# Performance work log

Hardware: AMD Instinct MI355X
Metric: run time of the kernel (lower is better)

Reference implementation:

```python
import jax, jax.numpy as jnp
import numpy as np

DIM = 256
HEADS = 8
HEAD_DIM = DIM // HEADS
SCALE = HEAD_DIM ** -0.5
B, N = 2048, 49
NW = 64


def setup_inputs() -> dict:
    key = jax.random.key(0)
    ks = jax.random.split(key, 7)
    x = jax.random.normal(ks[0], (B, N, DIM), dtype=jnp.float32)
    mask = jax.random.normal(ks[1], (NW, N + 1, N + 1), dtype=jnp.float32)
    class_token = 0.02 * jax.random.normal(ks[2], (1, 1, DIM), dtype=jnp.float32)
    qkv_w = jax.random.normal(ks[3], (DIM, 3 * DIM), dtype=jnp.float32) / np.sqrt(DIM)
    qkv_b = jnp.zeros((3 * DIM,), dtype=jnp.float32)
    proj_w = jax.random.normal(ks[4], (DIM, DIM), dtype=jnp.float32) / np.sqrt(DIM)
    proj_b = jnp.zeros((DIM,), dtype=jnp.float32)
    return {"x": x, "mask": mask, "class_token": class_token,
            "qkv_w": qkv_w, "qkv_b": qkv_b, "proj_w": proj_w, "proj_b": proj_b}


def reference(x, mask, class_token, qkv_w, qkv_b, proj_w, proj_b):
    b, n, c = x.shape
    n1 = n + 1
    # prepend learnable class token
    cls = jnp.broadcast_to(class_token, (b, 1, c))
    xc = jnp.concatenate([cls, x], axis=1)  # (B, N+1, C)
    # fused qkv projection
    qkv = xc @ qkv_w + qkv_b                 # (B, N+1, 3C)
    qkv = qkv.reshape(b, n1, 3, HEADS, HEAD_DIM)
    qkv = jnp.transpose(qkv, (2, 0, 3, 1, 4))  # (3, B, H, N+1, Dh)
    q, k, v = qkv[0] * SCALE, qkv[1], qkv[2]
    attn = jnp.einsum('bhid,bhjd->bhij', q, k)  # (B, H, N+1, N+1)
    # per-window additive mask bias
    nw = mask.shape[0]
    attn = attn.reshape(b // nw, nw, HEADS, n1, n1) + mask[None, :, None]
    attn = attn.reshape(b, HEADS, n1, n1)
    attn = jax.nn.softmax(attn, axis=-1)
    out = jnp.einsum('bhij,bhjd->bhid', attn, v)      # (B, H, N+1, Dh)
    out = jnp.transpose(out, (0, 2, 1, 3)).reshape(b, n1, c)
    out = out @ proj_w + proj_b
    return out[:, 0], out[:, 1:]
```

## Files before the change

### kernel.cpp

```cpp
#include <hip/hip_runtime.h>

#define NB    2048
#define N1    50
#define DIMC  256
#define NHEAD 8

typedef short  s16x8 __attribute__((ext_vector_type(8)));
typedef short  s16x4 __attribute__((ext_vector_type(4)));
typedef float  f32x4 __attribute__((ext_vector_type(4)));
typedef float  f32x2 __attribute__((ext_vector_type(2)));

__device__ __forceinline__ unsigned short f2bf(float f) {
    unsigned int u = __builtin_bit_cast(unsigned int, f);
    u = (u + 0x7FFFu + ((u >> 16) & 1u)) >> 16;
    return (unsigned short)u;
}
__device__ __forceinline__ s16x8 ld8(const unsigned short* p) {
    return *(const s16x8*)p;
}
__device__ __forceinline__ void gll16(const unsigned short* g, unsigned short* l) {
    __builtin_amdgcn_global_load_lds(
        (const __attribute__((address_space(1))) unsigned int*)g,
        (__attribute__((address_space(3))) unsigned int*)l, 16, 0, 0);
}

__global__ void prep_kernel(const float* __restrict__ qkv_w, const float* __restrict__ proj_w,
                            const float* __restrict__ mask,
                            unsigned short* __restrict__ wqkvB, unsigned short* __restrict__ wprojB,
                            float* __restrict__ maskP) {
    int idx = blockIdx.x * 256 + threadIdx.x;
    {
        int wv = idx >> 12, q = (idx >> 6) & 63, k = idx & 63;
        float v = (k < 50) ? ((q < 50) ? mask[(wv * 50 + q) * 50 + k] : 0.f) : -1e30f;
        maskP[idx] = v;
    }
    if (idx < 196608) {
        int ks = idx / 24576, rem = idx - ks * 24576, n = rem >> 5, kk = rem & 31;
        wqkvB[idx] = f2bf(qkv_w[(ks * 32 + kk) * 768 + n]);
    }
    if (idx < 65536) {
        int ks = idx >> 13, rem = idx & 8191, n = rem >> 5, kk = rem & 31;
        wprojB[idx] = f2bf(proj_w[(ks * 32 + kk) * 256 + n]);
    }
}

__global__ __launch_bounds__(1024, 4) void attn_kernel(
        const float* __restrict__ x, const float* __restrict__ cls,
        const float* __restrict__ qkv_b, const unsigned short* __restrict__ wqkvB,
        const float* __restrict__ maskP, unsigned short* __restrict__ attO) {
    __shared__ __align__(16) char smem_raw[155648];
    unsigned short* S   = (unsigned short*)smem_raw;
    unsigned short* sQ  = S;
    unsigned short* sK  = S + 20480;
    unsigned short* sVT = S + 40960;
    unsigned short* sP  = S + 59392;
    unsigned short* sXC = S;
    unsigned short* sB0 = S + 16896;
    unsigned short* sB1 = S + 41472;

    const int b = blockIdx.x, tid = threadIdx.x;
    const int lane = tid & 63, w = tid >> 6;
    const int ln15 = lane & 15, quad = lane >> 4, q8 = quad * 8;
    const int wm = w & 1, wn = w >> 1;
    const int win = b & 63;
    const float SCALE = 0.17677669529663687f;

    #pragma unroll
    for (int i = 0; i < 8; ++i) {
        int p = i * 1024 + tid;
        int r = p >> 7, c = (p & 127) * 2;
        float v0, v1;
        if (r == 0)       { v0 = cls[c]; v1 = cls[c + 1]; }
        else if (r <= 49) { const float* px = &x[((size_t)b * 49 + (r - 1)) * 256 + c];
                            f32x2 t = *(const f32x2*)px; v0 = t[0]; v1 = t[1]; }
        else              { v0 = 0.f; v1 = 0.f; }
        *(unsigned int*)&sXC[r * 264 + c] = (unsigned int)f2bf(v0) | ((unsigned int)f2bf(v1) << 16);
    }
    #pragma unroll
    for (int i = 0; i < 3; ++i) {
        int sb = w * 192 + i * 64;
        gll16(wqkvB + (sb + lane) * 8, sB0 + sb * 8);
    }
    __syncthreads();

    f32x4 acc[2][6];
    #pragma unroll
    for (int mt = 0; mt < 2; ++mt)
        #pragma unroll
        for (int nt = 0; nt < 6; ++nt) acc[mt][nt] = f32x4{0.f, 0.f, 0.f, 0.f};

    for (int ks = 0; ks < 8; ++ks) {
        unsigned short* bb = (ks & 1) ? sB1 : sB0;
        if (ks < 7) {
            unsigned short* nb = (ks & 1) ? sB0 : sB1;
            const unsigned short* src = wqkvB + (ks + 1) * 24576;
            #pragma unroll
            for (int i = 0; i < 3; ++i) {
                int sb = w * 192 + i * 64;
                gll16(src + (sb + lane) * 8, nb + sb * 8);
            }
        }
        s16x8 af[2], bf[6];
        #pragma unroll
        for (int mt = 0; mt < 2; ++mt)
            af[mt] = ld8(&sXC[(wm * 32 + mt * 16 + ln15) * 264 + ks * 32 + q8]);
        #pragma unroll
        for (int nt = 0; nt < 6; ++nt)
            bf[nt] = ld8(&bb[(wn * 96 + nt * 16 + ln15) * 32 + q8]);
        #pragma unroll
        for (int mt = 0; mt < 2; ++mt)
            #pragma unroll
            for (int nt = 0; nt < 6; ++nt)
                acc[mt][nt] = __builtin_amdgcn_mfma_f32_16x16x32_bf16(af[mt], bf[nt], acc[mt][nt], 0, 0, 0);
        __syncthreads();
    }

    #pragma unroll
    for (int mt = 0; mt < 2; ++mt) {
        const int tokb = wm * 32 + mt * 16 + quad * 4;
        #pragma unroll
        for (int nt = 0; nt < 6; ++nt) {
            const int gc = wn * 96 + nt * 16 + ln15;
            const int type = gc >> 8;
            const int hd = (gc >> 5) & 7, dd = gc & 31;
            const float bias = qkv_b[gc];
            if (type == 0) {
                #pragma unroll
                for (int i = 0; i < 4; ++i)
                    sQ[hd * 2560 + (tokb + i) * 40 + dd] = f2bf((acc[mt][nt][i] + bias) * SCALE);
            } else if (type == 1) {
                #pragma unroll
                for (int i = 0; i < 4; ++i)
                    sK[hd * 2560 + (tokb + i) * 40 + dd] = f2bf(acc[mt][nt][i] + bias);
            } else {
                s16x4 pk;
                #pragma unroll
                for (int i = 0; i < 4; ++i) pk[i] = f2bf(acc[mt][nt][i] + bias);
                *(s16x4*)&sVT[hd * 2304 + dd * 72 + tokb] = pk;
            }
        }
    }
    __syncthreads();

    const int h = w >> 1, rh = w & 1, qt0 = rh * 2;
    unsigned short* sPw = sP + w * 1152;

    s16x8 ak[4];
    #pragma unroll
    for (int kt = 0; kt < 4; ++kt)
        ak[kt] = ld8(&sK[h * 2560 + (kt * 16 + ln15) * 40 + q8]);

    f32x4 st[2][4];
    #pragma unroll
    for (int mt = 0; mt < 2; ++mt) {
        s16x8 bq = ld8(&sQ[h * 2560 + ((qt0 + mt) * 16 + ln15) * 40 + q8]);
        #pragma unroll
        for (int kt = 0; kt < 4; ++kt) {
            f32x4 z = {0.f, 0.f, 0.f, 0.f};
            st[mt][kt] = __builtin_amdgcn_mfma_f32_16x16x32_bf16(ak[kt], bq, z, 0, 0, 0);
        }
    }
    s16x8 pb[2][2];
    #pragma unroll
    for (int mt = 0; mt < 2; ++mt) {
        float sum = 0.f;
        #pragma unroll
        for (int kt = 0; kt < 4; ++kt) {
            f32x4 mk = *(const f32x4*)&maskP[((size_t)(win * 64 + (qt0 + mt) * 16 + ln15)) * 64 + kt * 16 + quad * 4];
            #pragma unroll
            for (int i = 0; i < 4; ++i) {
                float e = __expf(st[mt][kt][i] + mk[i]);
                st[mt][kt][i] = e;
                sum += e;
            }
        }
        sum += __shfl_xor(sum, 16, 64);
        sum += __shfl_xor(sum, 32, 64);
        const float inv = 1.f / sum;
        #pragma unroll
        for (int kt = 0; kt < 4; ++kt) {
            s16x4 pk;
            #pragma unroll
            for (int i = 0; i < 4; ++i) pk[i] = f2bf(st[mt][kt][i] * inv);
            *(s16x4*)&sPw[ln15 * 72 + kt * 16 + quad * 4] = pk;
        }
        asm volatile("s_waitcnt lgkmcnt(0)" ::: "memory");
        pb[mt][0] = ld8(&sPw[ln15 * 72 + q8]);
        pb[mt][1] = ld8(&sPw[ln15 * 72 + 32 + q8]);
    }
    s16x8 av[2][2];
    #pragma unroll
    for (int dt = 0; dt < 2; ++dt)
        #pragma unroll
        for (int kk = 0; kk < 2; ++kk)
            av[dt][kk] = ld8(&sVT[h * 2304 + (dt * 16 + ln15) * 72 + kk * 32 + q8]);
    f32x4 o[2][2];
    #pragma unroll
    for (int mt = 0; mt < 2; ++mt)
        #pragma unroll
        for (int dt = 0; dt < 2; ++dt) o[mt][dt] = f32x4{0.f, 0.f, 0.f, 0.f};
    #pragma unroll
    for (int mt = 0; mt < 2; ++mt)
        #pragma unroll
        for (int dt = 0; dt < 2; ++dt)
            #pragma unroll
            for (int kk = 0; kk < 2; ++kk)
                o[mt][dt] = __builtin_amdgcn_mfma_f32_16x16x32_bf16(av[dt][kk], pb[mt][kk], o[mt][dt], 0, 0, 0);
    #pragma unroll
    for (int mt = 0; mt < 2; ++mt) {
        const int qg = (qt0 + mt) * 16 + ln15;
        if (qg < N1) {
            #pragma unroll
            for (int dt = 0; dt < 2; ++dt) {
                s16x4 pk;
                #pragma unroll
                for (int i = 0; i < 4; ++i) pk[i] = f2bf(o[mt][dt][i]);
                *(s16x4*)&attO[((size_t)b * N1 + qg) * 256 + h * 32 + dt * 16 + quad * 4] = pk;
            }
        }
    }
}

__global__ __launch_bounds__(512, 4) void proj_kernel(
        const unsigned short* __restrict__ attO, const unsigned short* __restrict__ wprojB,
        const float* __restrict__ proj_b, float* __restrict__ out) {
    __shared__ __align__(16) char smem_raw[49152];
    unsigned short* S   = (unsigned short*)smem_raw;
    unsigned short* sA0 = S;
    unsigned short* sA1 = S + 4096;
    unsigned short* sB0 = S + 8192;
    unsigned short* sB1 = S + 16384;

    const int blk = blockIdx.x, tid = threadIdx.x;
    const int lane = tid & 63, w = tid >> 6;
    const int ln15 = lane & 15, quad = lane >> 4, q8 = quad * 8;
    const int wm = w >> 1, wn = w & 1;
    const size_t rbase = (size_t)blk * 128;

    const int s   = w * 64 + lane;
    const int arow = s >> 2, apart = s & 3;

    {
        gll16(attO + (rbase + arow) * 256 + apart * 8, sA0 + (w * 64) * 8);
        #pragma unroll
        for (int i = 0; i < 2; ++i) {
            int sb = i * 512 + w * 64;
            gll16(wprojB + (sb + lane) * 8, sB0 + sb * 8);
        }
    }
    __syncthreads();

    f32x4 acc[2][8];
    #pragma unroll
    for (int mt = 0; mt < 2; ++mt)
        #pragma unroll
        for (int nt = 0; nt < 8; ++nt) acc[mt][nt] = f32x4{0.f, 0.f, 0.f, 0.f};

    for (int ks = 0; ks < 8; ++ks) {
        unsigned short* a = (ks & 1) ? sA1 : sA0;
        unsigned short* bbuf = (ks & 1) ? sB1 : sB0;
        if (ks < 7) {
            unsigned short* na = (ks & 1) ? sA0 : sA1;
            unsigned short* nb = (ks & 1) ? sB0 : sB1;
            gll16(attO + (rbase + arow) * 256 + (ks + 1) * 32 + apart * 8, na + (w * 64) * 8);
            const unsigned short* src = wprojB + (ks + 1) * 8192;
            #pragma unroll
            for (int i = 0; i < 2; ++i) {
                int sb = i * 512 + w * 64;
                gll16(src + (sb + lane) * 8, nb + sb * 8);
            }
        }
        s16x8 af[2], bf[8];
        #pragma unroll
        for (int mt = 0; mt < 2; ++mt)
            af[mt] = ld8(&a[(wm * 32 + mt * 16 + ln15) * 32 + q8]);
        #pragma unroll
        for (int nt = 0; nt < 8; ++nt)
            bf[nt] = ld8(&bbuf[(wn * 128 + nt * 16 + ln15) * 32 + q8]);
        #pragma unroll
        for (int mt = 0; mt < 2; ++mt)
            #pragma unroll
            for (int nt = 0; nt < 8; ++nt)
                acc[mt][nt] = __builtin_amdgcn_mfma_f32_16x16x32_bf16(af[mt], bf[nt], acc[mt][nt], 0, 0, 0);
        __syncthreads();
    }

    #pragma unroll
    for (int mt = 0; mt < 2; ++mt) {
        #pragma unroll
        for (int nt = 0; nt < 8; ++nt) {
            const int gc = wn * 128 + nt * 16 + ln15;
            const float bias = proj_b[gc];
            #pragma unroll
            for (int i = 0; i < 4; ++i) {
                unsigned int R = (unsigned int)rbase + wm * 32 + mt * 16 + quad * 4 + i;
                unsigned int bidx = R / 50u, t = R % 50u;
                float v = acc[mt][nt][i] + bias;
                if (t == 0) out[(size_t)bidx * 256 + gc] = v;
                else        out[(size_t)524288 + ((size_t)bidx * 49 + (t - 1)) * 256 + gc] = v;
            }
        }
    }
}

extern "C" void kernel_launch(void* const* d_in, const int* in_sizes, int n_in,
                              void* d_out, int out_size, void* d_ws, size_t ws_size,
                              hipStream_t stream) {
    const float* x      = (const float*)d_in[0];
    const float* mask   = (const float*)d_in[1];
    const float* cls    = (const float*)d_in[2];
    const float* qkv_w  = (const float*)d_in[3];
    const float* qkv_b  = (const float*)d_in[4];
    const float* proj_w = (const float*)d_in[5];
    const float* proj_b = (const float*)d_in[6];
    float* out = (float*)d_out;

    unsigned short* attO   = (unsigned short*)d_ws;
    unsigned short* wqkvB  = (unsigned short*)((char*)d_ws + 52428800);
    unsigned short* wprojB = (unsigned short*)((char*)d_ws + 52822016);
    float*          maskP  = (float*)((char*)d_ws + 52953088);

    prep_kernel<<<1024, 256, 0, stream>>>(qkv_w, proj_w, mask, wqkvB, wprojB, maskP);
    attn_kernel<<<NB, 1024, 0, stream>>>(x, cls, qkv_b, wqkvB, maskP, attO);
    proj_kernel<<<800, 512, 0, stream>>>(attO, wprojB, proj_b, out);
}
```

Baseline: 318.5 us.

## Fuse output projection into attention kernel and load weights directly to registers

Merges the separate projection kernel into the attention kernel, so the attention output stays in shared memory (reusing the x buffer) instead of going to a global bf16 intermediate and back. Weight tiles for both GEMMs are now loaded straight from global memory into registers with register double-buffering, replacing the LDS staging and per-step barriers. The QKV GEMM warp tiling changes to 4x3 tiles per wave over all 64 rows, and P reuses the Q buffer region. In exchange, weights are re-read from L2 by every block per wave without LDS sharing, and the projection GEMM on 64 padded rows runs inside the large-block kernel.

```diff
diff --git a/kernel.cpp b/kernel.cpp
--- a/kernel.cpp
+++ b/kernel.cpp
@@ -17,11 +17,6 @@
 }
 __device__ __forceinline__ s16x8 ld8(const unsigned short* p) {
     return *(const s16x8*)p;
-}
-__device__ __forceinline__ void gll16(const unsigned short* g, unsigned short* l) {
-    __builtin_amdgcn_global_load_lds(
-        (const __attribute__((address_space(1))) unsigned int*)g,
-        (__attribute__((address_space(3))) unsigned int*)l, 16, 0, 0);
 }
 
 __global__ void prep_kernel(const float* __restrict__ qkv_w, const float* __restrict__ proj_w,
@@ -44,24 +39,21 @@
     }
 }
 
-__global__ __launch_bounds__(1024, 4) void attn_kernel(
+__global__ __launch_bounds__(1024, 4) void fused_kernel(
         const float* __restrict__ x, const float* __restrict__ cls,
         const float* __restrict__ qkv_b, const unsigned short* __restrict__ wqkvB,
-        const float* __restrict__ maskP, unsigned short* __restrict__ attO) {
-    __shared__ __align__(16) char smem_raw[155648];
+        const unsigned short* __restrict__ wprojB, const float* __restrict__ proj_b,
+        const float* __restrict__ maskP, float* __restrict__ out) {
+    __shared__ __align__(16) char smem_raw[152576];
     unsigned short* S   = (unsigned short*)smem_raw;
-    unsigned short* sQ  = S;
-    unsigned short* sK  = S + 20480;
-    unsigned short* sVT = S + 40960;
-    unsigned short* sP  = S + 59392;
     unsigned short* sXC = S;
-    unsigned short* sB0 = S + 16896;
-    unsigned short* sB1 = S + 41472;
+    unsigned short* sQ  = S + 16896;
+    unsigned short* sK  = S + 37376;
+    unsigned short* sVT = S + 57856;
 
     const int b = blockIdx.x, tid = threadIdx.x;
     const int lane = tid & 63, w = tid >> 6;
     const int ln15 = lane & 15, quad = lane >> 4, q8 = quad * 8;
-    const int wm = w & 1, wn = w >> 1;
     const int win = b & 63;
     const float SCALE = 0.17677669529663687f;
 
@@ -76,228 +68,198 @@
         else              { v0 = 0.f; v1 = 0.f; }
         *(unsigned int*)&sXC[r * 264 + c] = (unsigned int)f2bf(v0) | ((unsigned int)f2bf(v1) << 16);
     }
-    #pragma unroll
-    for (int i = 0; i < 3; ++i) {
-        int sb = w * 192 + i * 64;
-        gll16(wqkvB + (sb + lane) * 8, sB0 + sb * 8);
-    }
+    s16x8 bcur[3];
+    #pragma unroll
+    for (int nt = 0; nt < 3; ++nt)
+        bcur[nt] = ld8(wqkvB + (w * 48 + nt * 16 + ln15) * 32 + q8);
     __syncthreads();
 
-    f32x4 acc[2][6];
-    #pragma unroll
-    for (int mt = 0; mt < 2; ++mt)
-        #pragma unroll
-        for (int nt = 0; nt < 6; ++nt) acc[mt][nt] = f32x4{0.f, 0.f, 0.f, 0.f};
-
+    f32x4 acc[4][3];
+    #pragma unroll
+    for (int mt = 0; mt < 4; ++mt)
+        #pragma unroll
+        for (int nt = 0; nt < 3; ++nt) acc[mt][nt] = f32x4{0.f, 0.f, 0.f, 0.f};
+
+    #pragma unroll
     for (int ks = 0; ks < 8; ++ks) {
-        unsigned short* bb = (ks & 1) ? sB1 : sB0;
+        s16x8 bnext[3];
         if (ks < 7) {
-            unsigned short* nb = (ks & 1) ? sB0 : sB1;
             const unsigned short* src = wqkvB + (ks + 1) * 24576;
             #pragma unroll
-            for (int i = 0; i < 3; ++i) {
-                int sb = w * 192 + i * 64;
-                gll16(src + (sb + lane) * 8, nb + sb * 8);
-            }
-        }
-        s16x8 af[2], bf[6];
+            for (int nt = 0; nt < 3; ++nt)
+                bnext[nt] = ld8(src + (w * 48 + nt * 16 + ln15) * 32 + q8);
+        }
+        s16x8 af[4];
+        #pragma unroll
+        for (int mt = 0; mt < 4; ++mt)
+            af[mt] = ld8(&sXC[(mt * 16 + ln15) * 264 + ks * 32 + q8]);
+        #pragma unroll
+        for (int mt = 0; mt < 4; ++mt)
+            #pragma unroll
+            for (int nt = 0; nt < 3; ++nt)
+                acc[mt][nt] = __builtin_amdgcn_mfma_f32_16x16x32_bf16(af[mt], bcur[nt], acc[mt][nt], 0, 0, 0);
+        if (ks < 7) {
+            #pragma unroll
+            for (int nt = 0; nt < 3; ++nt) bcur[nt] = bnext[nt];
+        }
+    }
+
+    #pragma unroll
+    for (int nt = 0; nt < 3; ++nt) {
+        const int gc = w * 48 + nt * 16 + ln15;
+        const int type = (w * 48 + nt * 16) >> 8;
+        const int hd = (gc >> 5) & 7, dd = gc & 31;
+        const float bias = qkv_b[gc];
+        if (type == 0) {
+            #pragma unroll
+            for (int mt = 0; mt < 4; ++mt)
+                #pragma unroll
+                for (int i = 0; i < 4; ++i)
+                    sQ[hd * 2560 + (mt * 16 + quad * 4 + i) * 40 + dd] = f2bf((acc[mt][nt][i] + bias) * SCALE);
+        } else if (type == 1) {
+            #pragma unroll
+            for (int mt = 0; mt < 4; ++mt)
+                #pragma unroll
+                for (int i = 0; i < 4; ++i)
+                    sK[hd * 2560 + (mt * 16 + quad * 4 + i) * 40 + dd] = f2bf(acc[mt][nt][i] + bias);
+        } else {
+            #pragma unroll
+            for (int mt = 0; mt < 4; ++mt) {
+                s16x4 pk;
+                #pragma unroll
+                for (int i = 0; i < 4; ++i) pk[i] = f2bf(acc[mt][nt][i] + bias);
+                *(s16x4*)&sVT[hd * 2304 + dd * 72 + mt * 16 + quad * 4] = pk;
+            }
+        }
+    }
+    __syncthreads();
+
+    {
+        const int h = w >> 1, rh = w & 1, qt0 = rh * 2;
+        unsigned short* sPw = sQ + h * 2560 + rh * 1280;
+
+        s16x8 ak[4];
+        #pragma unroll
+        for (int kt = 0; kt < 4; ++kt)
+            ak[kt] = ld8(&sK[h * 2560 + (kt * 16 + ln15) * 40 + q8]);
+
+        f32x4 st[2][4];
+        #pragma unroll
+        for (int mt = 0; mt < 2; ++mt) {
+            s16x8 bq = ld8(&sQ[h * 2560 + ((qt0 + mt) * 16 + ln15) * 40 + q8]);
+            #pragma unroll
+            for (int kt = 0; kt < 4; ++kt) {
+                f32x4 z = {0.f, 0.f, 0.f, 0.f};
+                st[mt][kt] = __builtin_amdgcn_mfma_f32_16x16x32_bf16(ak[kt], bq, z, 0, 0, 0);
+            }
+        }
+        s16x8 pb[2][2];
+        #pragma unroll
+        for (int mt = 0; mt < 2; ++mt) {
+            float sum = 0.f;
+            #pragma unroll
+            for (int kt = 0; kt < 4; ++kt) {
+                f32x4 mk = *(const f32x4*)&maskP[((size_t)(win * 64 + (qt0 + mt) * 16 + ln15)) * 64 + kt * 16 + quad * 4];
+                #pragma unroll
+                for (int i = 0; i < 4; ++i) {
+                    float e = __expf(st[mt][kt][i] + mk[i]);
+                    st[mt][kt][i] = e;
+                    sum += e;
+                }
+            }
+            sum += __shfl_xor(sum, 16, 64);
+            sum += __shfl_xor(sum, 32, 64);
+            const float inv = 1.f / sum;
+            #pragma unroll
+            for (int kt = 0; kt < 4; ++kt) {
+                s16x4 pk;
+                #pragma unroll
+                for (int i = 0; i < 4; ++i) pk[i] = f2bf(st[mt][kt][i] * inv);
+                *(s16x4*)&sPw[ln15 * 72 + kt * 16 + quad * 4] = pk;
+            }
+            asm volatile("s_waitcnt lgkmcnt(0)" ::: "memory");
+            pb[mt][0] = ld8(&sPw[ln15 * 72 + q8]);
+            pb[mt][1] = ld8(&sPw[ln15 * 72 + 32 + q8]);
+        }
+        s16x8 av[2][2];
+        #pragma unroll
+        for (int dt = 0; dt < 2; ++dt)
+            #pragma unroll
+            for (int kk = 0; kk < 2; ++kk)
+                av[dt][kk] = ld8(&sVT[h * 2304 + (dt * 16 + ln15) * 72 + kk * 32 + q8]);
+        f32x4 o[2][2];
         #pragma unroll
         for (int mt = 0; mt < 2; ++mt)
-            af[mt] = ld8(&sXC[(wm * 32 + mt * 16 + ln15) * 264 + ks * 32 + q8]);
-        #pragma unroll
-        for (int nt = 0; nt < 6; ++nt)
-            bf[nt] = ld8(&bb[(wn * 96 + nt * 16 + ln15) * 32 + q8]);
+            #pragma unroll
+            for (int dt = 0; dt < 2; ++dt) o[mt][dt] = f32x4{0.f, 0.f, 0.f, 0.f};
         #pragma unroll
         for (int mt = 0; mt < 2; ++mt)
             #pragma unroll
-            for (int nt = 0; nt < 6; ++nt)
-                acc[mt][nt] = __builtin_amdgcn_mfma_f32_16x16x32_bf16(af[mt], bf[nt], acc[mt][nt], 0, 0, 0);
-        __syncthreads();
-    }
-
-    #pragma unroll
-    for (int mt = 0; mt < 2; ++mt) {
-        const int tokb = wm * 32 + mt * 16 + quad * 4;
-        #pragma unroll
-        for (int nt = 0; nt < 6; ++nt) {
-            const int gc = wn * 96 + nt * 16 + ln15;
-            const int type = gc >> 8;
-            const int hd = (gc >> 5) & 7, dd = gc & 31;
-            const float bias = qkv_b[gc];
-            if (type == 0) {
-                #pragma unroll
-                for (int i = 0; i < 4; ++i)
-                    sQ[hd * 2560 + (tokb + i) * 40 + dd] = f2bf((acc[mt][nt][i] + bias) * SCALE);
-            } else if (type == 1) {
-                #pragma unroll
-                for (int i = 0; i < 4; ++i)
-                    sK[hd * 2560 + (tokb + i) * 40 + dd] = f2bf(acc[mt][nt][i] + bias);
-            } else {
-                s16x4 pk;
-                #pragma unroll
-                for (int i = 0; i < 4; ++i) pk[i] = f2bf(acc[mt][nt][i] + bias);
-                *(s16x4*)&sVT[hd * 2304 + dd * 72 + tokb] = pk;
-            }
-        }
-    }
-    __syncthreads();
-
-    const int h = w >> 1, rh = w & 1, qt0 = rh * 2;
-    unsigned short* sPw = sP + w * 1152;
-
-    s16x8 ak[4];
-    #pragma unroll
-    for (int kt = 0; kt < 4; ++kt)
-        ak[kt] = ld8(&sK[h * 2560 + (kt * 16 + ln15) * 40 + q8]);
-
-    f32x4 st[2][4];
-    #pragma unroll
-    for (int mt = 0; mt < 2; ++mt) {
-        s16x8 bq = ld8(&sQ[h * 2560 + ((qt0 + mt) * 16 + ln15) * 40 + q8]);
-        #pragma unroll
-        for (int kt = 0; kt < 4; ++kt) {
-            f32x4 z = {0.f, 0.f, 0.f, 0.f};
-            st[mt][kt] = __builtin_amdgcn_mfma_f32_16x16x32_bf16(ak[kt], bq, z, 0, 0, 0);
-        }
-    }
-    s16x8 pb[2][2];
-    #pragma unroll
-    for (int mt = 0; mt < 2; ++mt) {
-        float sum = 0.f;
-        #pragma unroll
-        for (int kt = 0; kt < 4; ++kt) {
-            f32x4 mk = *(const f32x4*)&maskP[((size_t)(win * 64 + (qt0 + mt) * 16 + ln15)) * 64 + kt * 16 + quad * 4];
-            #pragma unroll
-            for (int i = 0; i < 4; ++i) {
-                float e = __expf(st[mt][kt][i] + mk[i]);
-                st[mt][kt][i] = e;
-                sum += e;
-            }
-        }
-        sum += __shfl_xor(sum, 16, 64);
-        sum += __shfl_xor(sum, 32, 64);
-        const float inv = 1.f / sum;
-        #pragma unroll
-        for (int kt = 0; kt < 4; ++kt) {
-            s16x4 pk;
-            #pragma unroll
-            for (int i = 0; i < 4; ++i) pk[i] = f2bf(st[mt][kt][i] * inv);
-            *(s16x4*)&sPw[ln15 * 72 + kt * 16 + quad * 4] = pk;
-        }
-        asm volatile("s_waitcnt lgkmcnt(0)" ::: "memory");
-        pb[mt][0] = ld8(&sPw[ln15 * 72 + q8]);
-        pb[mt][1] = ld8(&sPw[ln15 * 72 + 32 + q8]);
-    }
-    s16x8 av[2][2];
-    #pragma unroll
-    for (int dt = 0; dt < 2; ++dt)
-        #pragma unroll
-        for (int kk = 0; kk < 2; ++kk)
-            av[dt][kk] = ld8(&sVT[h * 2304 + (dt * 16 + ln15) * 72 + kk * 32 + q8]);
-    f32x4 o[2][2];
-    #pragma unroll
-    for (int mt = 0; mt < 2; ++mt)
-        #pragma unroll
-        for (int dt = 0; dt < 2; ++dt) o[mt][dt] = f32x4{0.f, 0.f, 0.f, 0.f};
-    #pragma unroll
-    for (int mt = 0; mt < 2; ++mt)
-        #pragma unroll
-        for (int dt = 0; dt < 2; ++dt)
-            #pragma unroll
-            for (int kk = 0; kk < 2; ++kk)
-                o[mt][dt] = __builtin_amdgcn_mfma_f32_16x16x32_bf16(av[dt][kk], pb[mt][kk], o[mt][dt], 0, 0, 0);
-    #pragma unroll
-    for (int mt = 0; mt < 2; ++mt) {
-        const int qg = (qt0 + mt) * 16 + ln15;
-        if (qg < N1) {
+            for (int dt = 0; dt < 2; ++dt)
+                #pragma unroll
+                for (int kk = 0; kk < 2; ++kk)
+                    o[mt][dt] = __builtin_amdgcn_mfma_f32_16x16x32_bf16(av[dt][kk], pb[mt][kk], o[mt][dt], 0, 0, 0);
+        #pragma unroll
+        for (int mt = 0; mt < 2; ++mt) {
+            const int qg = (qt0 + mt) * 16 + ln15;
             #pragma unroll
             for (int dt = 0; dt < 2; ++dt) {
                 s16x4 pk;
                 #pragma unroll
                 for (int i = 0; i < 4; ++i) pk[i] = f2bf(o[mt][dt][i]);
-                *(s16x4*)&attO[((size_t)b * N1 + qg) * 256 + h * 32 + dt * 16 + quad * 4] = pk;
-            }
-        }
-    }
-}
-
-__global__ __launch_bounds__(512, 4) void proj_kernel(
-        const unsigned short* __restrict__ attO, const unsigned short* __restrict__ wprojB,
-        const float* __restrict__ proj_b, float* __restrict__ out) {
-    __shared__ __align__(16) char smem_raw[49152];
-    unsigned short* S   = (unsigned short*)smem_raw;
-    unsigned short* sA0 = S;
-    unsigned short* sA1 = S + 4096;
-    unsigned short* sB0 = S + 8192;
-    unsigned short* sB1 = S + 16384;
-
-    const int blk = blockIdx.x, tid = threadIdx.x;
-    const int lane = tid & 63, w = tid >> 6;
-    const int ln15 = lane & 15, quad = lane >> 4, q8 = quad * 8;
-    const int wm = w >> 1, wn = w & 1;
-    const size_t rbase = (size_t)blk * 128;
-
-    const int s   = w * 64 + lane;
-    const int arow = s >> 2, apart = s & 3;
+                *(s16x4*)&sXC[qg * 264 + h * 32 + dt * 16 + quad * 4] = pk;
+            }
+        }
+    }
+    __syncthreads();
 
     {
-        gll16(attO + (rbase + arow) * 256 + apart * 8, sA0 + (w * 64) * 8);
-        #pragma unroll
-        for (int i = 0; i < 2; ++i) {
-            int sb = i * 512 + w * 64;
-            gll16(wprojB + (sb + lane) * 8, sB0 + sb * 8);
-        }
-    }
-    __syncthreads();
-
-    f32x4 acc[2][8];
-    #pragma unroll
-    for (int mt = 0; mt < 2; ++mt)
-        #pragma unroll
-        for (int nt = 0; nt < 8; ++nt) acc[mt][nt] = f32x4{0.f, 0.f, 0.f, 0.f};
-
-    for (int ks = 0; ks < 8; ++ks) {
-        unsigned short* a = (ks & 1) ? sA1 : sA0;
-        unsigned short* bbuf = (ks & 1) ? sB1 : sB0;
-        if (ks < 7) {
-            unsigned short* na = (ks & 1) ? sA0 : sA1;
-            unsigned short* nb = (ks & 1) ? sB0 : sB1;
-            gll16(attO + (rbase + arow) * 256 + (ks + 1) * 32 + apart * 8, na + (w * 64) * 8);
-            const unsigned short* src = wprojB + (ks + 1) * 8192;
-            #pragma unroll
-            for (int i = 0; i < 2; ++i) {
-                int sb = i * 512 + w * 64;
-                gll16(src + (sb + lane) * 8, nb + sb * 8);
-            }
-        }
-        s16x8 af[2], bf[8];
+        const int wm3 = w >> 3, wn3 = w & 7;
+        s16x8 b3[2];
+        #pragma unroll
+        for (int nt = 0; nt < 2; ++nt)
+            b3[nt] = ld8(wprojB + (wn3 * 32 + nt * 16 + ln15) * 32 + q8);
+        f32x4 a3[2][2];
         #pragma unroll
         for (int mt = 0; mt < 2; ++mt)
-            af[mt] = ld8(&a[(wm * 32 + mt * 16 + ln15) * 32 + q8]);
-        #pragma unroll
-        for (int nt = 0; nt < 8; ++nt)
-            bf[nt] = ld8(&bbuf[(wn * 128 + nt * 16 + ln15) * 32 + q8]);
-        #pragma unroll
-        for (int mt = 0; mt < 2; ++mt)
-            #pragma unroll
-            for (int nt = 0; nt < 8; ++nt)
-                acc[mt][nt] = __builtin_amdgcn_mfma_f32_16x16x32_bf16(af[mt], bf[nt], acc[mt][nt], 0, 0, 0);
-        __syncthreads();
-    }
-
-    #pragma unroll
-    for (int mt = 0; mt < 2; ++mt) {
-        #pragma unroll
-        for (int nt = 0; nt < 8; ++nt) {
-            const int gc = wn * 128 + nt * 16 + ln15;
+            #pragma unroll
+            for (int nt = 0; nt < 2; ++nt) a3[mt][nt] = f32x4{0.f, 0.f, 0.f, 0.f};
+        #pragma unroll
+        for (int ks = 0; ks < 8; ++ks) {
+            s16x8 b3n[2];
+            if (ks < 7) {
+                const unsigned short* src = wprojB + (ks + 1) * 8192;
+                #pragma unroll
+                for (int nt = 0; nt < 2; ++nt)
+                    b3n[nt] = ld8(src + (wn3 * 32 + nt * 16 + ln15) * 32 + q8);
+            }
+            s16x8 af3[2];
+            #pragma unroll
+            for (int mt = 0; mt < 2; ++mt)
+                af3[mt] = ld8(&sXC[(wm3 * 32 + mt * 16 + ln15) * 264 + ks * 32 + q8]);
+            #pragma unroll
+            for (int mt = 0; mt < 2; ++mt)
+                #pragma unroll
+                for (int nt = 0; nt < 2; ++nt)
+                    a3[mt][nt] = __builtin_amdgcn_mfma_f32_16x16x32_bf16(af3[mt], b3[nt], a3[mt][nt], 0, 0, 0);
+            if (ks < 7) {
+                #pragma unroll
+                for (int nt = 0; nt < 2; ++nt) b3[nt] = b3n[nt];
+            }
+        }
+        #pragma unroll
+        for (int nt = 0; nt < 2; ++nt) {
+            const int gc = wn3 * 32 + nt * 16 + ln15;
             const float bias = proj_b[gc];
             #pragma unroll
-            for (int i = 0; i < 4; ++i) {
-                unsigned int R = (unsigned int)rbase + wm * 32 + mt * 16 + quad * 4 + i;
-                unsigned int bidx = R / 50u, t = R % 50u;
-                float v = acc[mt][nt][i] + bias;
-                if (t == 0) out[(size_t)bidx * 256 + gc] = v;
-                else        out[(size_t)524288 + ((size_t)bidx * 49 + (t - 1)) * 256 + gc] = v;
+            for (int mt = 0; mt < 2; ++mt) {
+                #pragma unroll
+                for (int i = 0; i < 4; ++i) {
+                    const int t = wm3 * 32 + mt * 16 + quad * 4 + i;
+                    const float v = a3[mt][nt][i] + bias;
+                    if (t == 0)      out[(size_t)b * 256 + gc] = v;
+                    else if (t < 50) out[(size_t)524288 + ((size_t)b * 49 + (t - 1)) * 256 + gc] = v;
+                }
             }
         }
     }
@@ -315,12 +277,10 @@
     const float* proj_b = (const float*)d_in[6];
     float* out = (float*)d_out;
 
-    unsigned short* attO   = (unsigned short*)d_ws;
-    unsigned short* wqkvB  = (unsigned short*)((char*)d_ws + 52428800);
-    unsigned short* wprojB = (unsigned short*)((char*)d_ws + 52822016);
-    float*          maskP  = (float*)((char*)d_ws + 52953088);
+    unsigned short* wqkvB  = (unsigned short*)d_ws;
+    unsigned short* wprojB = (unsigned short*)((char*)d_ws + 393216);
+    float*          maskP  = (float*)((char*)d_ws + 524288);
 
     prep_kernel<<<1024, 256, 0, stream>>>(qkv_w, proj_w, mask, wqkvB, wprojB, maskP);
-    attn_kernel<<<NB, 1024, 0, stream>>>(x, cls, qkv_b, wqkvB, maskP, attO);
-    proj_kernel<<<800, 512, 0, stream>>>(attO, wprojB, proj_b, out);
-}
+    fused_kernel<<<NB, 1024, 0, stream>>>(x, cls, qkv_b, wqkvB, wprojB, proj_b, maskP, out);
+}
```

Result: faster. 311.2 us (-2.3%).
